# Performance work log

Hardware: AMD Instinct MI355X
Metric: run time of the kernel (lower is better)

The kernel has to match this reference:

```python
import jax, jax.numpy as jnp
import numpy as np

GAMMA = 0.1


def spmm(edge_index, edge_weight, feat, n_nodes):
    # y[dst] += w * feat[src]  -- sparse adjacency @ feat via gather/scatter
    src = edge_index[0]
    dst = edge_index[1]
    msgs = feat[src] * edge_weight[:, None]  # [E, d]
    return jax.ops.segment_sum(msgs, dst, num_segments=n_nodes)


def setup_inputs() -> dict:
    key = jax.random.key(0)
    ks = jax.random.split(key, 12)
    N, F, H, O = 50000, 500, 64, 16
    E, Ek = 1600000, 1000000
    x = jax.random.normal(ks[0], (N, F), dtype=jnp.float32)
    edge_index = jax.random.randint(ks[1], (2, E), 0, N, dtype=jnp.int32)
    edge_weight = jax.random.uniform(ks[2], (E,), dtype=jnp.float32)
    knn_edge_index = jax.random.randint(ks[3], (2, Ek), 0, N, dtype=jnp.int32)
    knn_edge_weight = jax.random.uniform(ks[4], (Ek,), dtype=jnp.float32)
    # glorot-ish scaled params
    W0 = jax.random.normal(ks[5], (F, H), dtype=jnp.float32) * (1.0 / np.sqrt(F))
    W1 = jax.random.normal(ks[6], (H, O), dtype=jnp.float32) * (1.0 / np.sqrt(H))
    score0 = jax.random.normal(ks[7], (F, 1), dtype=jnp.float32) * (1.0 / np.sqrt(F))
    score1 = jax.random.normal(ks[8], (H, 1), dtype=jnp.float32) * (1.0 / np.sqrt(H))
    Dk0 = jax.random.normal(ks[9], (F, 1), dtype=jnp.float32) * (1.0 / np.sqrt(F))
    Dk1 = jax.random.normal(ks[10], (H, 1), dtype=jnp.float32) * (1.0 / np.sqrt(H))
    z = jnp.zeros((1,), dtype=jnp.float32)
    return {
        "x": x, "edge_index": edge_index, "edge_weight": edge_weight,
        "knn_edge_index": knn_edge_index, "knn_edge_weight": knn_edge_weight,
        "W0": W0, "W1": W1,
        "score0": score0, "sbias0": z, "score1": score1, "sbias1": z,
        "Dk0": Dk0, "Dbias0": z, "Dk1": Dk1, "Dbias1": z,
    }


def reference(x, edge_index, edge_weight, knn_edge_index, knn_edge_weight,
              W0, W1, score0, sbias0, score1, sbias1,
              Dk0, Dbias0, Dk1, Dbias1):
    N = x.shape[0]
    layers = [(W0, score0, sbias0, Dk0, Dbias0),
              (W1, score1, sbias1, Dk1, Dbias1)]
    for W, sc, sb, dkw, dkb in layers:
        s = jax.nn.sigmoid(x @ sc + sb)          # [N, 1] gate
        Dk = x @ dkw + dkb                        # [N, 1] degree-like scale
        xW = x @ W                                # shared linear transform
        agg = spmm(edge_index, edge_weight, xW, N)        # GCNConv(x, adj)
        agg_knn = spmm(knn_edge_index, knn_edge_weight, xW, N)  # GCNConv(x, adj_knn)
        # acts are identity (acts=[None] and final act None); dropout off (eval)
        x = s * agg + (1.0 - s) * agg_knn + GAMMA * Dk * xW
    return x
```

## Files before the change

kernel.cpp:

```cpp
#include <hip/hip_runtime.h>
#include <math.h>

#define GAMMA 0.1f

typedef float f32x4 __attribute__((ext_vector_type(4)));
typedef short short4v __attribute__((ext_vector_type(4)));
typedef short short8 __attribute__((ext_vector_type(8)));

static __device__ __forceinline__ unsigned short f2bf(float f) {
  union { float f; unsigned u; } v; v.f = f;
  unsigned r = v.u + 0x7FFF + ((v.u >> 16) & 1);
  return (unsigned short)(r >> 16);
}
static __device__ __forceinline__ float bf2f(unsigned short b) {
  union { unsigned u; float f; } v; v.u = ((unsigned)b) << 16;
  return v.f;
}

__global__ __launch_bounds__(256) void setup_fused(
    int* __restrict__ bcnt2, int ncnt,
    const float* __restrict__ W0, const float* __restrict__ sc0,
    const float* __restrict__ dk0, unsigned short* __restrict__ Bt0, int F,
    const float* __restrict__ W1, const float* __restrict__ sc1,
    const float* __restrict__ dk1, unsigned short* __restrict__ Bt1) {
  int b = blockIdx.x;
  int t = threadIdx.x;
  if (b < 2) {
    int i = b * 256 + t;
    if (i < ncnt) bcnt2[i] = 0;
  } else if (b < 162) {
    int i = (b - 2) * 256 + t;
    int c = i >> 9;
    int k = i & 511;
    float v = 0.f;
    if (k < F) {
      if (c < 64) v = W0[(size_t)k * 64 + c];
      else if (c == 64) v = sc0[k];
      else if (c == 65) v = dk0[k];
    }
    Bt0[(size_t)((k >> 3) * 80 + c) * 8 + (k & 7)] = f2bf(v);
  } else {
    int i = (b - 162) * 256 + t;
    int c = i >> 6;
    int k = i & 63;
    float v;
    if (c < 16) v = W1[(size_t)k * 16 + c];
    else if (c == 16) v = sc1[k];
    else if (c == 17) v = dk1[k];
    else v = 0.f;
    Bt1[(size_t)((k >> 3) * 32 + c) * 8 + (k & 7)] = f2bf(v);
  }
}

template <int CFRAGS, int OUTFRAGS, int COLS>
__global__ __launch_bounds__(256) void mfma_linear_l0(
    const float* __restrict__ A, const unsigned short* __restrict__ Bt3,
    const float* __restrict__ sb, const float* __restrict__ db,
    unsigned short* __restrict__ outW, float* __restrict__ s,
    float* __restrict__ Dk, int N, int Kact) {
  constexpr int KPAD = 512;
  constexpr int KSPLIT = 4, RPB = 16;
  constexpr int KS_PER = (KPAD / 32) / KSPLIT;
  constexpr int H = OUTFRAGS * 16;
  __shared__ unsigned short Ald[RPB * KPAD];
  __shared__ float red[(KSPLIT - 1) * 64 * CFRAGS * 4];

  const int t = threadIdx.x;
  const int rowBase = blockIdx.x * RPB;

#pragma unroll
  for (int it = 0; it < (RPB * KPAD) / (256 * 4); ++it) {
    int li = it * 1024 + t * 4;
    int row = li >> 9;
    int col = li & 511;
    int grow = rowBase + row;
    f32x4 v = (f32x4)0.f;
    if (grow < N && col < Kact)
      v = *(const f32x4*)(A + (size_t)grow * Kact + col);
    short4v b;
#pragma unroll
    for (int j = 0; j < 4; ++j) b[j] = (short)f2bf(v[j]);
    int byte = row * (KPAD * 2) + ((col * 2) ^ ((row & 7) << 4));
    *(short4v*)((char*)Ald + byte) = b;
  }
  __syncthreads();

  const int kslice = t >> 6;
  const int l = t & 63;
  const int kgrp = l >> 4;
  const int lc = l & 15;
  const int lrow = lc;
  const int rowD = rowBase + kgrp * 4;

  f32x4 acc[CFRAGS];
#pragma unroll
  for (int i = 0; i < CFRAGS; ++i) acc[i] = (f32x4)0.f;

  const int rbyte = lrow * (KPAD * 2);
  const int rswz = (lrow & 7) << 4;
#pragma unroll
  for (int kk = 0; kk < KS_PER; ++kk) {
    const int ks = kslice * KS_PER + kk;
    short8 av = *(const short8*)((char*)Ald +
                                 (rbyte + ((ks * 64 + kgrp * 16) ^ rswz)));
    const unsigned short* bbase =
        Bt3 + (size_t)((ks * 4 + kgrp) * COLS + lc) * 8;
#pragma unroll
    for (int fc = 0; fc < CFRAGS; ++fc) {
      short8 bv = *(const short8*)(bbase + fc * 128);
      acc[fc] = __builtin_amdgcn_mfma_f32_16x16x32_bf16(av, bv, acc[fc], 0, 0, 0);
    }
  }

  if (kslice > 0) {
    float* dst = red + ((kslice - 1) * 64 + l) * (CFRAGS * 4);
#pragma unroll
    for (int fc = 0; fc < CFRAGS; ++fc)
#pragma unroll
      for (int r = 0; r < 4; ++r) dst[fc * 4 + r] = acc[fc][r];
  }
  __syncthreads();
  if (kslice == 0) {
#pragma unroll
    for (int s2 = 1; s2 < KSPLIT; ++s2) {
      const float* src2 = red + ((s2 - 1) * 64 + l) * (CFRAGS * 4);
#pragma unroll
      for (int fc = 0; fc < CFRAGS; ++fc)
#pragma unroll
        for (int r = 0; r < 4; ++r) acc[fc][r] += src2[fc * 4 + r];
    }
#pragma unroll
    for (int fc = 0; fc < OUTFRAGS; ++fc) {
#pragma unroll
      for (int r = 0; r < 4; ++r) {
        int gr = rowD + r;
        if (gr < N) outW[(size_t)gr * H + fc * 16 + lc] = f2bf(acc[fc][r]);
      }
    }
    if (lc < 2) {
      f32x4 g = acc[CFRAGS - 1];
#pragma unroll
      for (int r = 0; r < 4; ++r) {
        int gr = rowD + r;
        if (gr < N) {
          if (lc == 0) s[gr] = 1.f / (1.f + expf(-(g[r] + sb[0])));
          else Dk[gr] = g[r] + db[0];
        }
      }
    }
  }
}

template <int KPAD, int CFRAGS, int OUTFRAGS, int COLS>
__global__ __launch_bounds__(256) void mfma_linear_bf(
    const unsigned short* __restrict__ Aptr, const unsigned short* __restrict__ Bt3,
    const float* __restrict__ sb, const float* __restrict__ db,
    unsigned short* __restrict__ outW, float* __restrict__ s,
    float* __restrict__ Dk, int N, int Kact) {
  constexpr int H = OUTFRAGS * 16;
  constexpr int KSPLIT = 2, RG = 2, RPB = 32;
  constexpr int KS_PER = (KPAD / 32) / KSPLIT;
  __shared__ float red[(KSPLIT - 1) * RG * 64 * CFRAGS * 4];

  const int w = threadIdx.x >> 6;
  const int rowgrp = w % RG;
  const int kslice = w / RG;
  const int l = threadIdx.x & 63;
  const int kgrp = l >> 4;
  const int lc = l & 15;
  const int rowA = blockIdx.x * RPB + rowgrp * 16 + lc;
  const int rowD = blockIdx.x * RPB + rowgrp * 16 + kgrp * 4;
  const int rowSafe = (rowA < N) ? rowA : 0;

  f32x4 acc[CFRAGS];
#pragma unroll
  for (int i = 0; i < CFRAGS; ++i) acc[i] = (f32x4)0.f;

#pragma unroll
  for (int kk = 0; kk < KS_PER; ++kk) {
    const int ks = kslice * KS_PER + kk;
    const int kb = ks * 32 + kgrp * 8;
    short8 av = *(const short8*)(Aptr + (size_t)rowSafe * Kact + kb);
    const unsigned short* bbase =
        Bt3 + (size_t)((ks * 4 + kgrp) * COLS + lc) * 8;
#pragma unroll
    for (int fc = 0; fc < CFRAGS; ++fc) {
      short8 bv = *(const short8*)(bbase + fc * 128);
      acc[fc] = __builtin_amdgcn_mfma_f32_16x16x32_bf16(av, bv, acc[fc], 0, 0, 0);
    }
  }

  if (kslice > 0) {
    float* dst = red + ((rowgrp)*64 + l) * (CFRAGS * 4);
#pragma unroll
    for (int fc = 0; fc < CFRAGS; ++fc)
#pragma unroll
      for (int r = 0; r < 4; ++r) dst[fc * 4 + r] = acc[fc][r];
  }
  __syncthreads();
  if (kslice == 0) {
    const float* src2 = red + ((rowgrp)*64 + l) * (CFRAGS * 4);
#pragma unroll
    for (int fc = 0; fc < CFRAGS; ++fc)
#pragma unroll
      for (int r = 0; r < 4; ++r) acc[fc][r] += src2[fc * 4 + r];

#pragma unroll
    for (int fc = 0; fc < OUTFRAGS; ++fc) {
#pragma unroll
      for (int r = 0; r < 4; ++r) {
        int gr = rowD + r;
        if (gr < N) outW[(size_t)gr * H + fc * 16 + lc] = f2bf(acc[fc][r]);
      }
    }
    if (lc < 2) {
      f32x4 g = acc[CFRAGS - 1];
#pragma unroll
      for (int r = 0; r < 4; ++r) {
        int gr = rowD + r;
        if (gr < N) {
          if (lc == 0) s[gr] = 1.f / (1.f + expf(-(g[r] + sb[0])));
          else Dk[gr] = g[r] + db[0];
        }
      }
    }
  }
}

#define BIN_CHUNK 8192

__global__ __launch_bounds__(512) void bucket_count2(
    const int* __restrict__ eiA, int EA, int* __restrict__ bcntA,
    const int* __restrict__ eiK, int EK, int* __restrict__ bcntK, int nchA,
    int* __restrict__ pcnt) {
  const int* ei;
  int E, chunk;
  int* bcnt;
  if (blockIdx.x < nchA) { ei = eiA; E = EA; bcnt = bcntA; chunk = blockIdx.x; }
  else { ei = eiK; E = EK; bcnt = bcntK; chunk = blockIdx.x - nchA; }
  __shared__ int lc[256];
  if (threadIdx.x < 256) lc[threadIdx.x] = 0;
  __syncthreads();
  const int base = chunk * BIN_CHUNK;
  for (int k = threadIdx.x; k < BIN_CHUNK; k += 512) {
    int e = base + k;
    if (e < E) atomicAdd(&lc[ei[E + e] >> 8], 1);
  }
  __syncthreads();
  if (threadIdx.x < 256) {
    int c = lc[threadIdx.x];
    pcnt[blockIdx.x * 256 + threadIdx.x] = c;
    if (c) atomicAdd(&bcnt[threadIdx.x], c);
  }
}

__global__ __launch_bounds__(512) void bucket_scan2(
    int* __restrict__ bcntA, int* __restrict__ boffA, int* __restrict__ gcurA,
    int* __restrict__ bcntK, int* __restrict__ boffK, int* __restrict__ gcurK,
    int nb) {
  int* bcnt = blockIdx.x ? bcntK : bcntA;
  int* boff = blockIdx.x ? boffK : boffA;
  int* gcur = blockIdx.x ? gcurK : gcurA;
  __shared__ int sh[512];
  int t = threadIdx.x;
  int v = (t < nb) ? bcnt[t] : 0;
  sh[t] = v;
  __syncthreads();
  int acc = v;
  for (int off = 1; off < 512; off <<= 1) {
    int xx = (t >= off) ? sh[t - off] : 0;
    __syncthreads();
    acc += xx;
    sh[t] = acc;
    __syncthreads();
  }
  if (t < nb) {
    boff[t] = acc - v;
    gcur[t] = acc - v;
  }
  if (t == nb - 1) boff[nb] = acc;
}

__global__ __launch_bounds__(512) void bin_fill2(
    const int* __restrict__ eiA, const float* __restrict__ ewA, int EA,
    int* __restrict__ gcurA, int2* __restrict__ recA,
    const int* __restrict__ eiK, const float* __restrict__ ewK, int EK,
    int* __restrict__ gcurK, int2* __restrict__ recK, int nchA,
    const int* __restrict__ pcnt) {
  const int* ei;
  const float* ew;
  int E, chunk;
  int* gcur;
  int2* rec;
  if (blockIdx.x < nchA) {
    ei = eiA; ew = ewA; E = EA; gcur = gcurA; rec = recA; chunk = blockIdx.x;
  } else {
    ei = eiK; ew = ewK; E = EK; gcur = gcurK; rec = recK;
    chunk = blockIdx.x - nchA;
  }
  __shared__ int scur[256];
  if (threadIdx.x < 256) {
    int c = pcnt[blockIdx.x * 256 + threadIdx.x];
    scur[threadIdx.x] = c ? atomicAdd(&gcur[threadIdx.x], c) : 0;
  }
  __syncthreads();
  const int base = chunk * BIN_CHUNK;
  for (int k = threadIdx.x; k < BIN_CHUNK; k += 512) {
    int e = base + k;
    if (e < E) {
      int src = ei[e];
      int dst = ei[E + e];
      int pos = atomicAdd(&scur[dst >> 8], 1);
      rec[pos] = make_int2(((dst & 255) << 16) | src, __float_as_int(ew[e]));
    }
  }
}

__global__ __launch_bounds__(512) void tile_sort2(
    const int2* __restrict__ recRawA, const int* __restrict__ boffA,
    unsigned* __restrict__ recSA, int* __restrict__ rpA,
    const int2* __restrict__ recRawK, const int* __restrict__ boffK,
    unsigned* __restrict__ recSK, int* __restrict__ rpK, int N, int nb) {
  const int2* recRaw;
  const int* boff;
  unsigned* recS;
  int* rp;
  int tile;
  if (blockIdx.x < nb) {
    recRaw = recRawA; boff = boffA; recS = recSA; rp = rpA; tile = blockIdx.x;
  } else {
    recRaw = recRawK; boff = boffK; recS = recSK; rp = rpK;
    tile = blockIdx.x - nb;
  }
  __shared__ int cnt[256];
  __shared__ int sc[256];
  __shared__ int cur[256];
  const int lo = boff[tile], hi = boff[tile + 1];
  const int t = threadIdx.x;
  if (t < 256) cnt[t] = 0;
  __syncthreads();
  for (int j = lo + t; j < hi; j += 512)
    atomicAdd(&cnt[recRaw[j].x >> 16], 1);
  __syncthreads();
  if (t < 256) sc[t] = cnt[t];
  __syncthreads();
  for (int off = 1; off < 256; off <<= 1) {
    int v = 0;
    if (t < 256 && t >= off) v = sc[t - off];
    __syncthreads();
    if (t < 256) sc[t] += v;
    __syncthreads();
  }
  if (t < 256) {
    int excl = sc[t] - cnt[t];
    cur[t] = excl;
    int n = tile * 256 + t;
    if (n < N) rp[n] = lo + excl;
  }
  if (tile == nb - 1 && t == 0) rp[N] = hi;
  __syncthreads();
  for (int j = lo + t; j < hi; j += 512) {
    int2 r = recRaw[j];
    int pos = lo + atomicAdd(&cur[r.x >> 16], 1);
    recS[pos] = ((unsigned)f2bf(__int_as_float(r.y)) << 16) |
                (unsigned)(r.x & 0xFFFF);
  }
}

static __device__ __forceinline__ float gather64(
    const int* __restrict__ rp, const unsigned* __restrict__ rec,
    const unsigned short* __restrict__ feat, int n, int h) {
  int b = rp[n], e = rp[n + 1];
  float a[16];
#pragma unroll
  for (int u = 0; u < 16; ++u) a[u] = 0.f;
  int j = b;
  for (; j + 16 <= e; j += 16) {
#pragma unroll
    for (int u = 0; u < 16; ++u) {
      unsigned r = rec[j + u];
      a[u] += bf2f((unsigned short)(r >> 16)) *
              bf2f(feat[(size_t)(r & 0xFFFF) * 64 + h]);
    }
  }
  for (; j + 4 <= e; j += 4) {
#pragma unroll
    for (int u = 0; u < 4; ++u) {
      unsigned r = rec[j + u];
      a[u] += bf2f((unsigned short)(r >> 16)) *
              bf2f(feat[(size_t)(r & 0xFFFF) * 64 + h]);
    }
  }
  for (; j < e; ++j) {
    unsigned r = rec[j];
    a[0] += bf2f((unsigned short)(r >> 16)) *
            bf2f(feat[(size_t)(r & 0xFFFF) * 64 + h]);
  }
  float t0 = ((a[0] + a[1]) + (a[2] + a[3])) + ((a[4] + a[5]) + (a[6] + a[7]));
  float t1 = ((a[8] + a[9]) + (a[10] + a[11])) +
             ((a[12] + a[13]) + (a[14] + a[15]));
  return t0 + t1;
}

__global__ __launch_bounds__(256) void agg_combine64(
    const int* __restrict__ rpA, const unsigned* __restrict__ recA,
    const int* __restrict__ rpK, const unsigned* __restrict__ recK,
    const unsigned short* __restrict__ feat, const float* __restrict__ s,
    const float* __restrict__ Dk, unsigned short* __restrict__ outp, int N) {
  int n = __builtin_amdgcn_readfirstlane((blockIdx.x * 256 + threadIdx.x) >> 6);
  if (n >= N) return;
  int h = threadIdx.x & 63;
  float aA = gather64(rpA, recA, feat, n, h);
  float aK = gather64(rpK, recK, feat, n, h);
  float sv = s[n];
  float res = sv * aA + (1.f - sv) * aK +
              GAMMA * Dk[n] * bf2f(feat[(size_t)n * 64 + h]);
  outp[(size_t)n * 64 + h] = f2bf(res);
}

static __device__ __forceinline__ float gather16(
    const int* __restrict__ rp, const unsigned* __restrict__ rec,
    const unsigned short* __restrict__ feat, int n, int h) {
  int b = rp[n], e = rp[n + 1];
  float a0 = 0.f, a1 = 0.f, a2 = 0.f, a3 = 0.f;
  float a4 = 0.f, a5 = 0.f, a6 = 0.f, a7 = 0.f;
  int j = b;
  for (; j + 8 <= e; j += 8) {
    unsigned q0 = rec[j + 0];
    unsigned q1 = rec[j + 1];
    unsigned q2 = rec[j + 2];
    unsigned q3 = rec[j + 3];
    unsigned q4 = rec[j + 4];
    unsigned q5 = rec[j + 5];
    unsigned q6 = rec[j + 6];
    unsigned q7 = rec[j + 7];
    a0 += bf2f((unsigned short)(q0 >> 16)) *
          bf2f(feat[(size_t)(q0 & 0xFFFF) * 16 + h]);
    a1 += bf2f((unsigned short)(q1 >> 16)) *
          bf2f(feat[(size_t)(q1 & 0xFFFF) * 16 + h]);
    a2 += bf2f((unsigned short)(q2 >> 16)) *
          bf2f(feat[(size_t)(q2 & 0xFFFF) * 16 + h]);
    a3 += bf2f((unsigned short)(q3 >> 16)) *
          bf2f(feat[(size_t)(q3 & 0xFFFF) * 16 + h]);
    a4 += bf2f((unsigned short)(q4 >> 16)) *
          bf2f(feat[(size_t)(q4 & 0xFFFF) * 16 + h]);
    a5 += bf2f((unsigned short)(q5 >> 16)) *
          bf2f(feat[(size_t)(q5 & 0xFFFF) * 16 + h]);
    a6 += bf2f((unsigned short)(q6 >> 16)) *
          bf2f(feat[(size_t)(q6 & 0xFFFF) * 16 + h]);
    a7 += bf2f((unsigned short)(q7 >> 16)) *
          bf2f(feat[(size_t)(q7 & 0xFFFF) * 16 + h]);
  }
  for (; j < e; ++j) {
    unsigned q = rec[j];
    a0 += bf2f((unsigned short)(q >> 16)) *
          bf2f(feat[(size_t)(q & 0xFFFF) * 16 + h]);
  }
  return ((a0 + a1) + (a2 + a3)) + ((a4 + a5) + (a6 + a7));
}

__global__ __launch_bounds__(256) void agg_combine16(
    const int* __restrict__ rpA, const unsigned* __restrict__ recA,
    const int* __restrict__ rpK, const unsigned* __restrict__ recK,
    const unsigned short* __restrict__ feat, const float* __restrict__ s,
    const float* __restrict__ Dk, float* __restrict__ outp, int N) {
  int tid = blockIdx.x * 256 + threadIdx.x;
  int n = tid >> 4;
  int h = tid & 15;
  if (n >= N) return;
  float aA = gather16(rpA, recA, feat, n, h);
  float aK = gather16(rpK, recK, feat, n, h);
  float sv = s[n];
  float res = sv * aA + (1.f - sv) * aK +
              GAMMA * Dk[n] * bf2f(feat[(size_t)n * 16 + h]);
  outp[(size_t)n * 16 + h] = res;
}

extern "C" void kernel_launch(void* const* d_in, const int* in_sizes, int n_in,
                              void* d_out, int out_size, void* d_ws, size_t ws_size,
                              hipStream_t stream) {
  const float* x = (const float*)d_in[0];
  const int* edge_index = (const int*)d_in[1];
  const float* edge_weight = (const float*)d_in[2];
  const int* knn_edge_index = (const int*)d_in[3];
  const float* knn_edge_weight = (const float*)d_in[4];
  const float* W0 = (const float*)d_in[5];
  const float* W1 = (const float*)d_in[6];
  const float* score0 = (const float*)d_in[7];
  const float* sbias0 = (const float*)d_in[8];
  const float* score1 = (const float*)d_in[9];
  const float* sbias1 = (const float*)d_in[10];
  const float* Dk0 = (const float*)d_in[11];
  const float* Dbias0 = (const float*)d_in[12];
  const float* Dk1 = (const float*)d_in[13];
  const float* Dbias1 = (const float*)d_in[14];

  const int F = in_sizes[7];
  const int N = in_sizes[0] / F;
  const int E = in_sizes[2];
  const int Ek = in_sizes[4];
  (void)n_in; (void)ws_size; (void)out_size;

  const int nb = (N + 255) / 256;
  const int nchA = (E + BIN_CHUNK - 1) / BIN_CHUNK;
  const int nchK = (Ek + BIN_CHUNK - 1) / BIN_CHUNK;

  char* cur = (char*)d_ws;
  auto alloc = [&](size_t bytes) {
    char* p = cur;
    cur += (bytes + 255) & ~(size_t)255;
    return (void*)p;
  };
  float* sbuf = (float*)alloc((size_t)N * 4);
  float* dkbuf = (float*)alloc((size_t)N * 4);
  int* bcnt2 = (int*)alloc((size_t)2 * nb * 4);
  int* bcntA = bcnt2;
  int* bcntK = bcnt2 + nb;
  int* boffA = (int*)alloc((size_t)(nb + 1) * 4);
  int* boffK = (int*)alloc((size_t)(nb + 1) * 4);
  int* gcurA = (int*)alloc((size_t)nb * 4);
  int* gcurK = (int*)alloc((size_t)nb * 4);
  int* rpA = (int*)alloc((size_t)(N + 1) * 4);
  int* rpK = (int*)alloc((size_t)(N + 1) * 4);
  int* pcnt = (int*)alloc((size_t)(nchA + nchK) * 256 * 4);
  unsigned* recA = (unsigned*)alloc((size_t)E * 4);
  unsigned* recK = (unsigned*)alloc((size_t)Ek * 4);
  unsigned short* Bt0 = (unsigned short*)alloc((size_t)80 * 512 * 2);
  unsigned short* Bt1 = (unsigned short*)alloc((size_t)32 * 64 * 2);
  char* uni = (char*)alloc((size_t)(E + Ek) * 8);
  int2* recRawA = (int2*)uni;
  int2* recRawK = recRawA + E;
  unsigned short* xWb = (unsigned short*)uni;
  unsigned short* x1b = xWb + (size_t)N * 64;
  unsigned short* xW1b = x1b + (size_t)N * 64;

  const int gemmBlocksL0 = (N + 15) / 16;
  const int gemmBlocksL1 = (N + 31) / 32;
  const int agg64Blocks = (int)(((size_t)N * 64 + 255) / 256);
  const int agg16Blocks = (int)(((size_t)N * 16 + 255) / 256);

  setup_fused<<<170, 256, 0, stream>>>(bcnt2, 2 * nb, W0, score0, Dk0, Bt0, F,
                                       W1, score1, Dk1, Bt1);
  bucket_count2<<<nchA + nchK, 512, 0, stream>>>(edge_index, E, bcntA,
                                                 knn_edge_index, Ek, bcntK,
                                                 nchA, pcnt);
  bucket_scan2<<<2, 512, 0, stream>>>(bcntA, boffA, gcurA, bcntK, boffK,
                                      gcurK, nb);
  bin_fill2<<<nchA + nchK, 512, 0, stream>>>(edge_index, edge_weight, E,
                                             gcurA, recRawA, knn_edge_index,
                                             knn_edge_weight, Ek, gcurK,
                                             recRawK, nchA, pcnt);
  tile_sort2<<<2 * nb, 512, 0, stream>>>(recRawA, boffA, recA, rpA, recRawK,
                                         boffK, recK, rpK, N, nb);
  mfma_linear_l0<5, 4, 80><<<gemmBlocksL0, 256, 0, stream>>>(
      x, Bt0, sbias0, Dbias0, xWb, sbuf, dkbuf, N, F);
  agg_combine64<<<agg64Blocks, 256, 0, stream>>>(rpA, recA, rpK, recK, xWb,
                                                 sbuf, dkbuf, x1b, N);
  mfma_linear_bf<64, 2, 1, 32><<<gemmBlocksL1, 256, 0, stream>>>(
      x1b, Bt1, sbias1, Dbias1, xW1b, sbuf, dkbuf, N, 64);
  agg_combine16<<<agg16Blocks, 256, 0, stream>>>(rpA, recA, rpK, recK, xW1b,
                                                 sbuf, dkbuf, (float*)d_out, N);
}
```

Measured before the change: 169.0 us.

## Replace per-node CSR sort with tile-local LDS fixed-point atomic aggregation

Drops the tile_sort2 pass that built a per-node CSR. The bucketed raw edge records, now in 128-node tiles, are aggregated directly inside 1024-thread blocks. Each block accumulates messages into LDS with integer atomics on fixed-point scaled products, then applies the gate/Dk combine and writes the output. This removes a full sort pass over all edges and its record reads and writes. The cost is LDS atomic contention, fixed-point quantization and overflow risk, larger 8-byte records read twice, and separate allocations instead of the aliased workspace.

Result: slower. 236.1 us (+39.7%).

```diff
diff --git a/kernel.cpp b/kernel.cpp
--- a/kernel.cpp
+++ b/kernel.cpp
@@ -2,6 +2,10 @@
 #include <math.h>
 
 #define GAMMA 0.1f
+#define SCALE0 32768.0f
+#define INV0 (1.0f / 32768.0f)
+#define SCALE1 8192.0f
+#define INV1 (1.0f / 8192.0f)
 
 typedef float f32x4 __attribute__((ext_vector_type(4)));
 typedef short short4v __attribute__((ext_vector_type(4)));
@@ -25,11 +29,11 @@
     const float* __restrict__ dk1, unsigned short* __restrict__ Bt1) {
   int b = blockIdx.x;
   int t = threadIdx.x;
-  if (b < 2) {
+  if (b < 4) {
     int i = b * 256 + t;
     if (i < ncnt) bcnt2[i] = 0;
-  } else if (b < 162) {
-    int i = (b - 2) * 256 + t;
+  } else if (b < 164) {
+    int i = (b - 4) * 256 + t;
     int c = i >> 9;
     int k = i & 511;
     float v = 0.f;
@@ -40,7 +44,7 @@
     }
     Bt0[(size_t)((k >> 3) * 80 + c) * 8 + (k & 7)] = f2bf(v);
   } else {
-    int i = (b - 162) * 256 + t;
+    int i = (b - 164) * 256 + t;
     int c = i >> 6;
     int k = i & 63;
     float v;
@@ -238,18 +242,18 @@
   int* bcnt;
   if (blockIdx.x < nchA) { ei = eiA; E = EA; bcnt = bcntA; chunk = blockIdx.x; }
   else { ei = eiK; E = EK; bcnt = bcntK; chunk = blockIdx.x - nchA; }
-  __shared__ int lc[256];
-  if (threadIdx.x < 256) lc[threadIdx.x] = 0;
+  __shared__ int lc[512];
+  lc[threadIdx.x] = 0;
   __syncthreads();
   const int base = chunk * BIN_CHUNK;
   for (int k = threadIdx.x; k < BIN_CHUNK; k += 512) {
     int e = base + k;
-    if (e < E) atomicAdd(&lc[ei[E + e] >> 8], 1);
-  }
-  __syncthreads();
-  if (threadIdx.x < 256) {
+    if (e < E) atomicAdd(&lc[ei[E + e] >> 7], 1);
+  }
+  __syncthreads();
+  {
     int c = lc[threadIdx.x];
-    pcnt[blockIdx.x * 256 + threadIdx.x] = c;
+    pcnt[blockIdx.x * 512 + threadIdx.x] = c;
     if (c) atomicAdd(&bcnt[threadIdx.x], c);
   }
 }
@@ -298,9 +302,9 @@
     ei = eiK; ew = ewK; E = EK; gcur = gcurK; rec = recK;
     chunk = blockIdx.x - nchA;
   }
-  __shared__ int scur[256];
-  if (threadIdx.x < 256) {
-    int c = pcnt[blockIdx.x * 256 + threadIdx.x];
+  __shared__ int scur[512];
+  {
+    int c = pcnt[blockIdx.x * 512 + threadIdx.x];
     scur[threadIdx.x] = c ? atomicAdd(&gcur[threadIdx.x], c) : 0;
   }
   __syncthreads();
@@ -310,170 +314,180 @@
     if (e < E) {
       int src = ei[e];
       int dst = ei[E + e];
-      int pos = atomicAdd(&scur[dst >> 8], 1);
-      rec[pos] = make_int2(((dst & 255) << 16) | src, __float_as_int(ew[e]));
-    }
-  }
-}
-
-__global__ __launch_bounds__(512) void tile_sort2(
-    const int2* __restrict__ recRawA, const int* __restrict__ boffA,
-    unsigned* __restrict__ recSA, int* __restrict__ rpA,
-    const int2* __restrict__ recRawK, const int* __restrict__ boffK,
-    unsigned* __restrict__ recSK, int* __restrict__ rpK, int N, int nb) {
-  const int2* recRaw;
-  const int* boff;
-  unsigned* recS;
-  int* rp;
-  int tile;
-  if (blockIdx.x < nb) {
-    recRaw = recRawA; boff = boffA; recS = recSA; rp = rpA; tile = blockIdx.x;
-  } else {
-    recRaw = recRawK; boff = boffK; recS = recSK; rp = rpK;
-    tile = blockIdx.x - nb;
-  }
-  __shared__ int cnt[256];
-  __shared__ int sc[256];
-  __shared__ int cur[256];
-  const int lo = boff[tile], hi = boff[tile + 1];
-  const int t = threadIdx.x;
-  if (t < 256) cnt[t] = 0;
-  __syncthreads();
-  for (int j = lo + t; j < hi; j += 512)
-    atomicAdd(&cnt[recRaw[j].x >> 16], 1);
-  __syncthreads();
-  if (t < 256) sc[t] = cnt[t];
-  __syncthreads();
-  for (int off = 1; off < 256; off <<= 1) {
-    int v = 0;
-    if (t < 256 && t >= off) v = sc[t - off];
-    __syncthreads();
-    if (t < 256) sc[t] += v;
-    __syncthreads();
-  }
-  if (t < 256) {
-    int excl = sc[t] - cnt[t];
-    cur[t] = excl;
-    int n = tile * 256 + t;
-    if (n < N) rp[n] = lo + excl;
-  }
-  if (tile == nb - 1 && t == 0) rp[N] = hi;
-  __syncthreads();
-  for (int j = lo + t; j < hi; j += 512) {
-    int2 r = recRaw[j];
-    int pos = lo + atomicAdd(&cur[r.x >> 16], 1);
-    recS[pos] = ((unsigned)f2bf(__int_as_float(r.y)) << 16) |
-                (unsigned)(r.x & 0xFFFF);
-  }
-}
-
-static __device__ __forceinline__ float gather64(
-    const int* __restrict__ rp, const unsigned* __restrict__ rec,
-    const unsigned short* __restrict__ feat, int n, int h) {
-  int b = rp[n], e = rp[n + 1];
-  float a[16];
-#pragma unroll
-  for (int u = 0; u < 16; ++u) a[u] = 0.f;
-  int j = b;
-  for (; j + 16 <= e; j += 16) {
-#pragma unroll
-    for (int u = 0; u < 16; ++u) {
-      unsigned r = rec[j + u];
-      a[u] += bf2f((unsigned short)(r >> 16)) *
-              bf2f(feat[(size_t)(r & 0xFFFF) * 64 + h]);
-    }
-  }
-  for (; j + 4 <= e; j += 4) {
-#pragma unroll
-    for (int u = 0; u < 4; ++u) {
-      unsigned r = rec[j + u];
-      a[u] += bf2f((unsigned short)(r >> 16)) *
-              bf2f(feat[(size_t)(r & 0xFFFF) * 64 + h]);
-    }
-  }
-  for (; j < e; ++j) {
-    unsigned r = rec[j];
-    a[0] += bf2f((unsigned short)(r >> 16)) *
-            bf2f(feat[(size_t)(r & 0xFFFF) * 64 + h]);
-  }
-  float t0 = ((a[0] + a[1]) + (a[2] + a[3])) + ((a[4] + a[5]) + (a[6] + a[7]));
-  float t1 = ((a[8] + a[9]) + (a[10] + a[11])) +
-             ((a[12] + a[13]) + (a[14] + a[15]));
-  return t0 + t1;
-}
-
-__global__ __launch_bounds__(256) void agg_combine64(
-    const int* __restrict__ rpA, const unsigned* __restrict__ recA,
-    const int* __restrict__ rpK, const unsigned* __restrict__ recK,
+      int pos = atomicAdd(&scur[dst >> 7], 1);
+      rec[pos] = make_int2(((dst & 127) << 16) | src, __float_as_int(ew[e]));
+    }
+  }
+}
+
+__global__ __launch_bounds__(1024) void aggfix64(
+    const int2* __restrict__ rawA, const int* __restrict__ boffA,
+    const int2* __restrict__ rawK, const int* __restrict__ boffK,
     const unsigned short* __restrict__ feat, const float* __restrict__ s,
     const float* __restrict__ Dk, unsigned short* __restrict__ outp, int N) {
-  int n = __builtin_amdgcn_readfirstlane((blockIdx.x * 256 + threadIdx.x) >> 6);
-  if (n >= N) return;
-  int h = threadIdx.x & 63;
-  float aA = gather64(rpA, recA, feat, n, h);
-  float aK = gather64(rpK, recK, feat, n, h);
-  float sv = s[n];
-  float res = sv * aA + (1.f - sv) * aK +
-              GAMMA * Dk[n] * bf2f(feat[(size_t)n * 64 + h]);
-  outp[(size_t)n * 64 + h] = f2bf(res);
-}
-
-static __device__ __forceinline__ float gather16(
-    const int* __restrict__ rp, const unsigned* __restrict__ rec,
-    const unsigned short* __restrict__ feat, int n, int h) {
-  int b = rp[n], e = rp[n + 1];
-  float a0 = 0.f, a1 = 0.f, a2 = 0.f, a3 = 0.f;
-  float a4 = 0.f, a5 = 0.f, a6 = 0.f, a7 = 0.f;
-  int j = b;
-  for (; j + 8 <= e; j += 8) {
-    unsigned q0 = rec[j + 0];
-    unsigned q1 = rec[j + 1];
-    unsigned q2 = rec[j + 2];
-    unsigned q3 = rec[j + 3];
-    unsigned q4 = rec[j + 4];
-    unsigned q5 = rec[j + 5];
-    unsigned q6 = rec[j + 6];
-    unsigned q7 = rec[j + 7];
-    a0 += bf2f((unsigned short)(q0 >> 16)) *
-          bf2f(feat[(size_t)(q0 & 0xFFFF) * 16 + h]);
-    a1 += bf2f((unsigned short)(q1 >> 16)) *
-          bf2f(feat[(size_t)(q1 & 0xFFFF) * 16 + h]);
-    a2 += bf2f((unsigned short)(q2 >> 16)) *
-          bf2f(feat[(size_t)(q2 & 0xFFFF) * 16 + h]);
-    a3 += bf2f((unsigned short)(q3 >> 16)) *
-          bf2f(feat[(size_t)(q3 & 0xFFFF) * 16 + h]);
-    a4 += bf2f((unsigned short)(q4 >> 16)) *
-          bf2f(feat[(size_t)(q4 & 0xFFFF) * 16 + h]);
-    a5 += bf2f((unsigned short)(q5 >> 16)) *
-          bf2f(feat[(size_t)(q5 & 0xFFFF) * 16 + h]);
-    a6 += bf2f((unsigned short)(q6 >> 16)) *
-          bf2f(feat[(size_t)(q6 & 0xFFFF) * 16 + h]);
-    a7 += bf2f((unsigned short)(q7 >> 16)) *
-          bf2f(feat[(size_t)(q7 & 0xFFFF) * 16 + h]);
-  }
-  for (; j < e; ++j) {
-    unsigned q = rec[j];
-    a0 += bf2f((unsigned short)(q >> 16)) *
-          bf2f(feat[(size_t)(q & 0xFFFF) * 16 + h]);
-  }
-  return ((a0 + a1) + (a2 + a3)) + ((a4 + a5) + (a6 + a7));
-}
-
-__global__ __launch_bounds__(256) void agg_combine16(
-    const int* __restrict__ rpA, const unsigned* __restrict__ recA,
-    const int* __restrict__ rpK, const unsigned* __restrict__ recK,
+  __shared__ int acc[128 * 64];
+  const int tile = blockIdx.x;
+  const int node0 = tile * 128;
+  const int t = threadIdx.x;
+  const int wid = t >> 6;
+  const int h = t & 63;
+
+#pragma unroll
+  for (int u = 0; u < 8; ++u) acc[t + u * 1024] = 0;
+  __syncthreads();
+
+  {
+    int lo = boffA[tile], hi = boffA[tile + 1];
+    int per = (hi - lo + 15) >> 4;
+    int wb = lo + wid * per;
+    int we = min(wb + per, hi);
+    int j = wb;
+    for (; j + 4 <= we; j += 4) {
+      int2 r0 = rawA[j + 0];
+      int2 r1 = rawA[j + 1];
+      int2 r2 = rawA[j + 2];
+      int2 r3 = rawA[j + 3];
+      float f0 = bf2f(feat[(size_t)(r0.x & 0xFFFF) * 64 + h]);
+      float f1 = bf2f(feat[(size_t)(r1.x & 0xFFFF) * 64 + h]);
+      float f2 = bf2f(feat[(size_t)(r2.x & 0xFFFF) * 64 + h]);
+      float f3 = bf2f(feat[(size_t)(r3.x & 0xFFFF) * 64 + h]);
+      atomicAdd(&acc[((r0.x >> 16) & 127) * 64 + h],
+                __float2int_rn(__int_as_float(r0.y) * f0 * SCALE0));
+      atomicAdd(&acc[((r1.x >> 16) & 127) * 64 + h],
+                __float2int_rn(__int_as_float(r1.y) * f1 * SCALE0));
+      atomicAdd(&acc[((r2.x >> 16) & 127) * 64 + h],
+                __float2int_rn(__int_as_float(r2.y) * f2 * SCALE0));
+      atomicAdd(&acc[((r3.x >> 16) & 127) * 64 + h],
+                __float2int_rn(__int_as_float(r3.y) * f3 * SCALE0));
+    }
+    for (; j < we; ++j) {
+      int2 r = rawA[j];
+      float f = bf2f(feat[(size_t)(r.x & 0xFFFF) * 64 + h]);
+      atomicAdd(&acc[((r.x >> 16) & 127) * 64 + h],
+                __float2int_rn(__int_as_float(r.y) * f * SCALE0));
+    }
+  }
+  __syncthreads();
+
+  float keep[8];
+#pragma unroll
+  for (int u = 0; u < 8; ++u) {
+    int idx = t + u * 1024;
+    int n = node0 + (idx >> 6);
+    keep[u] = (n < N) ? s[n] * (float)acc[idx] * INV0 : 0.f;
+  }
+  __syncthreads();
+#pragma unroll
+  for (int u = 0; u < 8; ++u) acc[t + u * 1024] = 0;
+  __syncthreads();
+
+  {
+    int lo = boffK[tile], hi = boffK[tile + 1];
+    int per = (hi - lo + 15) >> 4;
+    int wb = lo + wid * per;
+    int we = min(wb + per, hi);
+    int j = wb;
+    for (; j + 4 <= we; j += 4) {
+      int2 r0 = rawK[j + 0];
+      int2 r1 = rawK[j + 1];
+      int2 r2 = rawK[j + 2];
+      int2 r3 = rawK[j + 3];
+      float f0 = bf2f(feat[(size_t)(r0.x & 0xFFFF) * 64 + h]);
+      float f1 = bf2f(feat[(size_t)(r1.x & 0xFFFF) * 64 + h]);
+      float f2 = bf2f(feat[(size_t)(r2.x & 0xFFFF) * 64 + h]);
+      float f3 = bf2f(feat[(size_t)(r3.x & 0xFFFF) * 64 + h]);
+      atomicAdd(&acc[((r0.x >> 16) & 127) * 64 + h],
+                __float2int_rn(__int_as_float(r0.y) * f0 * SCALE0));
+      atomicAdd(&acc[((r1.x >> 16) & 127) * 64 + h],
+                __float2int_rn(__int_as_float(r1.y) * f1 * SCALE0));
+      atomicAdd(&acc[((r2.x >> 16) & 127) * 64 + h],
+                __float2int_rn(__int_as_float(r2.y) * f2 * SCALE0));
+      atomicAdd(&acc[((r3.x >> 16) & 127) * 64 + h],
+                __float2int_rn(__int_as_float(r3.y) * f3 * SCALE0));
+    }
+    for (; j < we; ++j) {
+      int2 r = rawK[j];
+      float f = bf2f(feat[(size_t)(r.x & 0xFFFF) * 64 + h]);
+      atomicAdd(&acc[((r.x >> 16) & 127) * 64 + h],
+                __float2int_rn(__int_as_float(r.y) * f * SCALE0));
+    }
+  }
+  __syncthreads();
+
+#pragma unroll
+  for (int u = 0; u < 8; ++u) {
+    int idx = t + u * 1024;
+    int n = node0 + (idx >> 6);
+    int h2 = idx & 63;
+    if (n < N) {
+      float res = keep[u] + (1.f - s[n]) * (float)acc[idx] * INV0 +
+                  GAMMA * Dk[n] * bf2f(feat[(size_t)n * 64 + h2]);
+      outp[(size_t)n * 64 + h2] = f2bf(res);
+    }
+  }
+}
+
+__global__ __launch_bounds__(1024) void aggfix16(
+    const int2* __restrict__ rawA, const int* __restrict__ boffA,
+    const int2* __restrict__ rawK, const int* __restrict__ boffK,
     const unsigned short* __restrict__ feat, const float* __restrict__ s,
     const float* __restrict__ Dk, float* __restrict__ outp, int N) {
-  int tid = blockIdx.x * 256 + threadIdx.x;
-  int n = tid >> 4;
-  int h = tid & 15;
-  if (n >= N) return;
-  float aA = gather16(rpA, recA, feat, n, h);
-  float aK = gather16(rpK, recK, feat, n, h);
-  float sv = s[n];
-  float res = sv * aA + (1.f - sv) * aK +
-              GAMMA * Dk[n] * bf2f(feat[(size_t)n * 16 + h]);
-  outp[(size_t)n * 16 + h] = res;
+  __shared__ int accA[128 * 16];
+  __shared__ int accK[128 * 16];
+  const int tile = blockIdx.x;
+  const int node0 = tile * 128;
+  const int t = threadIdx.x;
+  const int wid = t >> 6;
+  const int lane = t & 63;
+  const int eg = lane >> 4;
+  const int h = lane & 15;
+
+#pragma unroll
+  for (int u = 0; u < 2; ++u) {
+    accA[t + u * 1024] = 0;
+    accK[t + u * 1024] = 0;
+  }
+  __syncthreads();
+
+  {
+    int lo = boffA[tile], hi = boffA[tile + 1];
+    int per = (hi - lo + 15) >> 4;
+    int wb = lo + wid * per;
+    int we = min(wb + per, hi);
+    for (int j = wb + eg; j < we; j += 4) {
+      int2 r = rawA[j];
+      float f = bf2f(feat[(size_t)(r.x & 0xFFFF) * 16 + h]);
+      atomicAdd(&accA[((r.x >> 16) & 127) * 16 + h],
+                __float2int_rn(__int_as_float(r.y) * f * SCALE1));
+    }
+  }
+  {
+    int lo = boffK[tile], hi = boffK[tile + 1];
+    int per = (hi - lo + 15) >> 4;
+    int wb = lo + wid * per;
+    int we = min(wb + per, hi);
+    for (int j = wb + eg; j < we; j += 4) {
+      int2 r = rawK[j];
+      float f = bf2f(feat[(size_t)(r.x & 0xFFFF) * 16 + h]);
+      atomicAdd(&accK[((r.x >> 16) & 127) * 16 + h],
+                __float2int_rn(__int_as_float(r.y) * f * SCALE1));
+    }
+  }
+  __syncthreads();
+
+#pragma unroll
+  for (int u = 0; u < 2; ++u) {
+    int idx = t + u * 1024;
+    int n = node0 + (idx >> 4);
+    int h2 = idx & 15;
+    if (n < N) {
+      float sv = s[n];
+      float res = sv * (float)accA[idx] * INV1 +
+                  (1.f - sv) * (float)accK[idx] * INV1 +
+                  GAMMA * Dk[n] * bf2f(feat[(size_t)n * 16 + h2]);
+      outp[(size_t)n * 16 + h2] = res;
+    }
+  }
 }
 
 extern "C" void kernel_launch(void* const* d_in, const int* in_sizes, int n_in,
@@ -501,7 +515,7 @@
   const int Ek = in_sizes[4];
   (void)n_in; (void)ws_size; (void)out_size;
 
-  const int nb = (N + 255) / 256;
+  const int nb = (N + 127) / 128;
   const int nchA = (E + BIN_CHUNK - 1) / BIN_CHUNK;
   const int nchK = (Ek + BIN_CHUNK - 1) / BIN_CHUNK;
 
@@ -520,26 +534,19 @@
   int* boffK = (int*)alloc((size_t)(nb + 1) * 4);
   int* gcurA = (int*)alloc((size_t)nb * 4);
   int* gcurK = (int*)alloc((size_t)nb * 4);
-  int* rpA = (int*)alloc((size_t)(N + 1) * 4);
-  int* rpK = (int*)alloc((size_t)(N + 1) * 4);
-  int* pcnt = (int*)alloc((size_t)(nchA + nchK) * 256 * 4);
-  unsigned* recA = (unsigned*)alloc((size_t)E * 4);
-  unsigned* recK = (unsigned*)alloc((size_t)Ek * 4);
+  int* pcnt = (int*)alloc((size_t)(nchA + nchK) * 512 * 4);
+  int2* recRawA = (int2*)alloc((size_t)E * 8);
+  int2* recRawK = (int2*)alloc((size_t)Ek * 8);
   unsigned short* Bt0 = (unsigned short*)alloc((size_t)80 * 512 * 2);
   unsigned short* Bt1 = (unsigned short*)alloc((size_t)32 * 64 * 2);
-  char* uni = (char*)alloc((size_t)(E + Ek) * 8);
-  int2* recRawA = (int2*)uni;
-  int2* recRawK = recRawA + E;
-  unsigned short* xWb = (unsigned short*)uni;
-  unsigned short* x1b = xWb + (size_t)N * 64;
-  unsigned short* xW1b = x1b + (size_t)N * 64;
+  unsigned short* xWb = (unsigned short*)alloc((size_t)N * 64 * 2);
+  unsigned short* x1b = (unsigned short*)alloc((size_t)N * 64 * 2);
+  unsigned short* xW1b = (unsigned short*)alloc((size_t)N * 16 * 2);
 
   const int gemmBlocksL0 = (N + 15) / 16;
   const int gemmBlocksL1 = (N + 31) / 32;
-  const int agg64Blocks = (int)(((size_t)N * 64 + 255) / 256);
-  const int agg16Blocks = (int)(((size_t)N * 16 + 255) / 256);
-
-  setup_fused<<<170, 256, 0, stream>>>(bcnt2, 2 * nb, W0, score0, Dk0, Bt0, F,
+
+  setup_fused<<<172, 256, 0, stream>>>(bcnt2, 2 * nb, W0, score0, Dk0, Bt0, F,
                                        W1, score1, Dk1, Bt1);
   bucket_count2<<<nchA + nchK, 512, 0, stream>>>(edge_index, E, bcntA,
                                                  knn_edge_index, Ek, bcntK,
@@ -550,14 +557,12 @@
                                              gcurA, recRawA, knn_edge_index,
                                              knn_edge_weight, Ek, gcurK,
                                              recRawK, nchA, pcnt);
-  tile_sort2<<<2 * nb, 512, 0, stream>>>(recRawA, boffA, recA, rpA, recRawK,
-                                         boffK, recK, rpK, N, nb);
   mfma_linear_l0<5, 4, 80><<<gemmBlocksL0, 256, 0, stream>>>(
       x, Bt0, sbias0, Dbias0, xWb, sbuf, dkbuf, N, F);
-  agg_combine64<<<agg64Blocks, 256, 0, stream>>>(rpA, recA, rpK, recK, xWb,
-                                                 sbuf, dkbuf, x1b, N);
+  aggfix64<<<nb, 1024, 0, stream>>>(recRawA, boffA, recRawK, boffK, xWb,
+                                    sbuf, dkbuf, x1b, N);
   mfma_linear_bf<64, 2, 1, 32><<<gemmBlocksL1, 256, 0, stream>>>(
       x1b, Bt1, sbias1, Dbias1, xW1b, sbuf, dkbuf, N, 64);
-  agg_combine16<<<agg16Blocks, 256, 0, stream>>>(rpA, recA, rpK, recK, xW1b,
-                                                 sbuf, dkbuf, (float*)d_out, N);
-}
+  aggfix16<<<nb, 1024, 0, stream>>>(recRawA, boffA, recRawK, boffK, xW1b,
+                                    sbuf, dkbuf, (float*)d_out, N);
+}
```

## Fuse bucket counting into prep kernel and split aggregation across graph wavefronts

Applied to the files above, without the earlier changes.

Bucket counting now runs inside the setup kernel, and the scan sums per-chunk counts itself, which removes one launch and the global bucket atomics. bin_fill also keeps a per-node degree count with global atomics, so tile_sort can skip its counting pass over the raw records. agg_combine64 now gives the adjacency gather and the kNN gather to separate wavefronts and combines them through shared memory, doubling parallelism per node. In exchange, bin_fill issues millions of global atomics and the aggregation adds a block-level barrier.

Measured after the change: 285.2 us. +68.7%, slower.

```diff
diff --git a/kernel.cpp b/kernel.cpp
--- a/kernel.cpp
+++ b/kernel.cpp
@@ -2,6 +2,7 @@
 #include <math.h>
 
 #define GAMMA 0.1f
+#define BIN_CHUNK 8192
 
 typedef float f32x4 __attribute__((ext_vector_type(4)));
 typedef short short4v __attribute__((ext_vector_type(4)));
@@ -17,19 +18,22 @@
   return v.f;
 }
 
-__global__ __launch_bounds__(256) void setup_fused(
-    int* __restrict__ bcnt2, int ncnt,
+__global__ __launch_bounds__(512) void prep_fused(
+    int* __restrict__ dcnt2, int nzero,
     const float* __restrict__ W0, const float* __restrict__ sc0,
     const float* __restrict__ dk0, unsigned short* __restrict__ Bt0, int F,
     const float* __restrict__ W1, const float* __restrict__ sc1,
-    const float* __restrict__ dk1, unsigned short* __restrict__ Bt1) {
-  int b = blockIdx.x;
-  int t = threadIdx.x;
-  if (b < 2) {
-    int i = b * 256 + t;
-    if (i < ncnt) bcnt2[i] = 0;
-  } else if (b < 162) {
-    int i = (b - 2) * 256 + t;
+    const float* __restrict__ dk1, unsigned short* __restrict__ Bt1,
+    const int* __restrict__ eiA, int EA, const int* __restrict__ eiK, int EK,
+    int nchA, int* __restrict__ pcnt, int ZB) {
+  __shared__ int lc[256];
+  const int b = blockIdx.x;
+  const int t = threadIdx.x;
+  if (b < ZB) {
+    int i = b * 512 + t;
+    if (i < nzero) dcnt2[i] = 0;
+  } else if (b < ZB + 80) {
+    int i = (b - ZB) * 512 + t;
     int c = i >> 9;
     int k = i & 511;
     float v = 0.f;
@@ -39,8 +43,8 @@
       else if (c == 65) v = dk0[k];
     }
     Bt0[(size_t)((k >> 3) * 80 + c) * 8 + (k & 7)] = f2bf(v);
-  } else {
-    int i = (b - 162) * 256 + t;
+  } else if (b < ZB + 84) {
+    int i = (b - ZB - 80) * 512 + t;
     int c = i >> 6;
     int k = i & 63;
     float v;
@@ -49,6 +53,145 @@
     else if (c == 17) v = dk1[k];
     else v = 0.f;
     Bt1[(size_t)((k >> 3) * 32 + c) * 8 + (k & 7)] = f2bf(v);
+  } else {
+    int ci = b - (ZB + 84);
+    const int* ei;
+    int E, chunk;
+    if (ci < nchA) { ei = eiA; E = EA; chunk = ci; }
+    else { ei = eiK; E = EK; chunk = ci - nchA; }
+    if (t < 256) lc[t] = 0;
+    __syncthreads();
+    const int base = chunk * BIN_CHUNK;
+    for (int k = t; k < BIN_CHUNK; k += 512) {
+      int e = base + k;
+      if (e < E) atomicAdd(&lc[ei[E + e] >> 8], 1);
+    }
+    __syncthreads();
+    if (t < 256) pcnt[(size_t)ci * 256 + t] = lc[t];
+  }
+}
+
+__global__ __launch_bounds__(512) void bucket_scan2(
+    const int* __restrict__ pcnt, int nchA, int nchK, int nb,
+    int* __restrict__ boffA, int* __restrict__ gcurA,
+    int* __restrict__ boffK, int* __restrict__ gcurK) {
+  const int* base = blockIdx.x ? (pcnt + (size_t)nchA * 256) : pcnt;
+  const int nch = blockIdx.x ? nchK : nchA;
+  int* boff = blockIdx.x ? boffK : boffA;
+  int* gcur = blockIdx.x ? gcurK : gcurA;
+  __shared__ int sh[512];
+  int t = threadIdx.x;
+  int v = 0;
+  if (t < nb)
+    for (int c = 0; c < nch; ++c) v += base[(size_t)c * 256 + t];
+  sh[t] = v;
+  __syncthreads();
+  int acc = v;
+  for (int off = 1; off < 512; off <<= 1) {
+    int xx = (t >= off) ? sh[t - off] : 0;
+    __syncthreads();
+    acc += xx;
+    sh[t] = acc;
+    __syncthreads();
+  }
+  if (t < nb) {
+    boff[t] = acc - v;
+    gcur[t] = acc - v;
+  }
+  if (t == nb - 1) boff[nb] = acc;
+}
+
+__global__ __launch_bounds__(512) void bin_fill2(
+    const int* __restrict__ eiA, const float* __restrict__ ewA, int EA,
+    int* __restrict__ gcurA, int2* __restrict__ recA,
+    const int* __restrict__ eiK, const float* __restrict__ ewK, int EK,
+    int* __restrict__ gcurK, int2* __restrict__ recK, int nchA,
+    const int* __restrict__ pcnt, int* __restrict__ dcntA,
+    int* __restrict__ dcntK) {
+  const int* ei;
+  const float* ew;
+  int E, chunk;
+  int* gcur;
+  int2* rec;
+  int* dcnt;
+  if (blockIdx.x < nchA) {
+    ei = eiA; ew = ewA; E = EA; gcur = gcurA; rec = recA; dcnt = dcntA;
+    chunk = blockIdx.x;
+  } else {
+    ei = eiK; ew = ewK; E = EK; gcur = gcurK; rec = recK; dcnt = dcntK;
+    chunk = blockIdx.x - nchA;
+  }
+  __shared__ int scur[256];
+  if (threadIdx.x < 256) {
+    int c = pcnt[(size_t)blockIdx.x * 256 + threadIdx.x];
+    scur[threadIdx.x] = c ? atomicAdd(&gcur[threadIdx.x], c) : 0;
+  }
+  __syncthreads();
+  const int base = chunk * BIN_CHUNK;
+  for (int k = threadIdx.x; k < BIN_CHUNK; k += 512) {
+    int e = base + k;
+    if (e < E) {
+      int src = ei[e];
+      int dst = ei[E + e];
+      int pos = atomicAdd(&scur[dst >> 8], 1);
+      rec[pos] = make_int2(((dst & 255) << 16) | src, __float_as_int(ew[e]));
+      atomicAdd(&dcnt[dst], 1);
+    }
+  }
+}
+
+__global__ __launch_bounds__(512) void tile_sort2(
+    const int2* __restrict__ recRawA, const int* __restrict__ boffA,
+    unsigned* __restrict__ recSA, int* __restrict__ rpA,
+    const int* __restrict__ dcntA,
+    const int2* __restrict__ recRawK, const int* __restrict__ boffK,
+    unsigned* __restrict__ recSK, int* __restrict__ rpK,
+    const int* __restrict__ dcntK, int N, int nb) {
+  const int2* recRaw;
+  const int* boff;
+  unsigned* recS;
+  int* rp;
+  const int* dcnt;
+  int tile;
+  if (blockIdx.x < nb) {
+    recRaw = recRawA; boff = boffA; recS = recSA; rp = rpA; dcnt = dcntA;
+    tile = blockIdx.x;
+  } else {
+    recRaw = recRawK; boff = boffK; recS = recSK; rp = rpK; dcnt = dcntK;
+    tile = blockIdx.x - nb;
+  }
+  __shared__ int cnt[256];
+  __shared__ int sc[256];
+  __shared__ int cur[256];
+  const int lo = boff[tile], hi = boff[tile + 1];
+  const int t = threadIdx.x;
+  if (t < 256) {
+    int nn = tile * 256 + t;
+    cnt[t] = (nn < N) ? dcnt[nn] : 0;
+  }
+  __syncthreads();
+  if (t < 256) sc[t] = cnt[t];
+  __syncthreads();
+  for (int off = 1; off < 256; off <<= 1) {
+    int v = 0;
+    if (t < 256 && t >= off) v = sc[t - off];
+    __syncthreads();
+    if (t < 256) sc[t] += v;
+    __syncthreads();
+  }
+  if (t < 256) {
+    int excl = sc[t] - cnt[t];
+    cur[t] = excl;
+    int n = tile * 256 + t;
+    if (n < N) rp[n] = lo + excl;
+  }
+  if (tile == nb - 1 && t == 0) rp[N] = hi;
+  __syncthreads();
+  for (int j = lo + t; j < hi; j += 512) {
+    int2 r = recRaw[j];
+    int pos = lo + atomicAdd(&cur[r.x >> 16], 1);
+    recS[pos] = ((unsigned)f2bf(__int_as_float(r.y)) << 16) |
+                (unsigned)(r.x & 0xFFFF);
   }
 }
 
@@ -227,146 +370,6 @@
   }
 }
 
-#define BIN_CHUNK 8192
-
-__global__ __launch_bounds__(512) void bucket_count2(
-    const int* __restrict__ eiA, int EA, int* __restrict__ bcntA,
-    const int* __restrict__ eiK, int EK, int* __restrict__ bcntK, int nchA,
-    int* __restrict__ pcnt) {
-  const int* ei;
-  int E, chunk;
-  int* bcnt;
-  if (blockIdx.x < nchA) { ei = eiA; E = EA; bcnt = bcntA; chunk = blockIdx.x; }
-  else { ei = eiK; E = EK; bcnt = bcntK; chunk = blockIdx.x - nchA; }
-  __shared__ int lc[256];
-  if (threadIdx.x < 256) lc[threadIdx.x] = 0;
-  __syncthreads();
-  const int base = chunk * BIN_CHUNK;
-  for (int k = threadIdx.x; k < BIN_CHUNK; k += 512) {
-    int e = base + k;
-    if (e < E) atomicAdd(&lc[ei[E + e] >> 8], 1);
-  }
-  __syncthreads();
-  if (threadIdx.x < 256) {
-    int c = lc[threadIdx.x];
-    pcnt[blockIdx.x * 256 + threadIdx.x] = c;
-    if (c) atomicAdd(&bcnt[threadIdx.x], c);
-  }
-}
-
-__global__ __launch_bounds__(512) void bucket_scan2(
-    int* __restrict__ bcntA, int* __restrict__ boffA, int* __restrict__ gcurA,
-    int* __restrict__ bcntK, int* __restrict__ boffK, int* __restrict__ gcurK,
-    int nb) {
-  int* bcnt = blockIdx.x ? bcntK : bcntA;
-  int* boff = blockIdx.x ? boffK : boffA;
-  int* gcur = blockIdx.x ? gcurK : gcurA;
-  __shared__ int sh[512];
-  int t = threadIdx.x;
-  int v = (t < nb) ? bcnt[t] : 0;
-  sh[t] = v;
-  __syncthreads();
-  int acc = v;
-  for (int off = 1; off < 512; off <<= 1) {
-    int xx = (t >= off) ? sh[t - off] : 0;
-    __syncthreads();
-    acc += xx;
-    sh[t] = acc;
-    __syncthreads();
-  }
-  if (t < nb) {
-    boff[t] = acc - v;
-    gcur[t] = acc - v;
-  }
-  if (t == nb - 1) boff[nb] = acc;
-}
-
-__global__ __launch_bounds__(512) void bin_fill2(
-    const int* __restrict__ eiA, const float* __restrict__ ewA, int EA,
-    int* __restrict__ gcurA, int2* __restrict__ recA,
-    const int* __restrict__ eiK, const float* __restrict__ ewK, int EK,
-    int* __restrict__ gcurK, int2* __restrict__ recK, int nchA,
-    const int* __restrict__ pcnt) {
-  const int* ei;
-  const float* ew;
-  int E, chunk;
-  int* gcur;
-  int2* rec;
-  if (blockIdx.x < nchA) {
-    ei = eiA; ew = ewA; E = EA; gcur = gcurA; rec = recA; chunk = blockIdx.x;
-  } else {
-    ei = eiK; ew = ewK; E = EK; gcur = gcurK; rec = recK;
-    chunk = blockIdx.x - nchA;
-  }
-  __shared__ int scur[256];
-  if (threadIdx.x < 256) {
-    int c = pcnt[blockIdx.x * 256 + threadIdx.x];
-    scur[threadIdx.x] = c ? atomicAdd(&gcur[threadIdx.x], c) : 0;
-  }
-  __syncthreads();
-  const int base = chunk * BIN_CHUNK;
-  for (int k = threadIdx.x; k < BIN_CHUNK; k += 512) {
-    int e = base + k;
-    if (e < E) {
-      int src = ei[e];
-      int dst = ei[E + e];
-      int pos = atomicAdd(&scur[dst >> 8], 1);
-      rec[pos] = make_int2(((dst & 255) << 16) | src, __float_as_int(ew[e]));
-    }
-  }
-}
-
-__global__ __launch_bounds__(512) void tile_sort2(
-    const int2* __restrict__ recRawA, const int* __restrict__ boffA,
-    unsigned* __restrict__ recSA, int* __restrict__ rpA,
-    const int2* __restrict__ recRawK, const int* __restrict__ boffK,
-    unsigned* __restrict__ recSK, int* __restrict__ rpK, int N, int nb) {
-  const int2* recRaw;
-  const int* boff;
-  unsigned* recS;
-  int* rp;
-  int tile;
-  if (blockIdx.x < nb) {
-    recRaw = recRawA; boff = boffA; recS = recSA; rp = rpA; tile = blockIdx.x;
-  } else {
-    recRaw = recRawK; boff = boffK; recS = recSK; rp = rpK;
-    tile = blockIdx.x - nb;
-  }
-  __shared__ int cnt[256];
-  __shared__ int sc[256];
-  __shared__ int cur[256];
-  const int lo = boff[tile], hi = boff[tile + 1];
-  const int t = threadIdx.x;
-  if (t < 256) cnt[t] = 0;
-  __syncthreads();
-  for (int j = lo + t; j < hi; j += 512)
-    atomicAdd(&cnt[recRaw[j].x >> 16], 1);
-  __syncthreads();
-  if (t < 256) sc[t] = cnt[t];
-  __syncthreads();
-  for (int off = 1; off < 256; off <<= 1) {
-    int v = 0;
-    if (t < 256 && t >= off) v = sc[t - off];
-    __syncthreads();
-    if (t < 256) sc[t] += v;
-    __syncthreads();
-  }
-  if (t < 256) {
-    int excl = sc[t] - cnt[t];
-    cur[t] = excl;
-    int n = tile * 256 + t;
-    if (n < N) rp[n] = lo + excl;
-  }
-  if (tile == nb - 1 && t == 0) rp[N] = hi;
-  __syncthreads();
-  for (int j = lo + t; j < hi; j += 512) {
-    int2 r = recRaw[j];
-    int pos = lo + atomicAdd(&cur[r.x >> 16], 1);
-    recS[pos] = ((unsigned)f2bf(__int_as_float(r.y)) << 16) |
-                (unsigned)(r.x & 0xFFFF);
-  }
-}
-
 static __device__ __forceinline__ float gather64(
     const int* __restrict__ rp, const unsigned* __restrict__ rec,
     const unsigned short* __restrict__ feat, int n, int h) {
@@ -407,15 +410,28 @@
     const int* __restrict__ rpK, const unsigned* __restrict__ recK,
     const unsigned short* __restrict__ feat, const float* __restrict__ s,
     const float* __restrict__ Dk, unsigned short* __restrict__ outp, int N) {
-  int n = __builtin_amdgcn_readfirstlane((blockIdx.x * 256 + threadIdx.x) >> 6);
-  if (n >= N) return;
-  int h = threadIdx.x & 63;
-  float aA = gather64(rpA, recA, feat, n, h);
-  float aK = gather64(rpK, recK, feat, n, h);
-  float sv = s[n];
-  float res = sv * aA + (1.f - sv) * aK +
-              GAMMA * Dk[n] * bf2f(feat[(size_t)n * 64 + h]);
-  outp[(size_t)n * 64 + h] = f2bf(res);
+  __shared__ float part[2][64];
+  const int t = threadIdx.x;
+  const int wid = t >> 6;
+  const int h = t & 63;
+  const int slot = wid >> 1;
+  const int graph = wid & 1;
+  int n = __builtin_amdgcn_readfirstlane(blockIdx.x * 2 + slot);
+
+  float mine = 0.f;
+  if (n < N)
+    mine = graph ? gather64(rpK, recK, feat, n, h)
+                 : gather64(rpA, recA, feat, n, h);
+  if (graph) part[slot][h] = mine;
+  __syncthreads();
+  if (n < N && graph == 0) {
+    float aA = mine;
+    float aK = part[slot][h];
+    float sv = s[n];
+    float res = sv * aA + (1.f - sv) * aK +
+                GAMMA * Dk[n] * bf2f(feat[(size_t)n * 64 + h]);
+    outp[(size_t)n * 64 + h] = f2bf(res);
+  }
 }
 
 static __device__ __forceinline__ float gather16(
@@ -504,6 +520,7 @@
   const int nb = (N + 255) / 256;
   const int nchA = (E + BIN_CHUNK - 1) / BIN_CHUNK;
   const int nchK = (Ek + BIN_CHUNK - 1) / BIN_CHUNK;
+  const int ZB = (2 * N + 511) / 512;
 
   char* cur = (char*)d_ws;
   auto alloc = [&](size_t bytes) {
@@ -513,9 +530,9 @@
   };
   float* sbuf = (float*)alloc((size_t)N * 4);
   float* dkbuf = (float*)alloc((size_t)N * 4);
-  int* bcnt2 = (int*)alloc((size_t)2 * nb * 4);
-  int* bcntA = bcnt2;
-  int* bcntK = bcnt2 + nb;
+  int* dcnt2 = (int*)alloc((size_t)2 * N * 4);
+  int* dcntA = dcnt2;
+  int* dcntK = dcnt2 + N;
   int* boffA = (int*)alloc((size_t)(nb + 1) * 4);
   int* boffK = (int*)alloc((size_t)(nb + 1) * 4);
   int* gcurA = (int*)alloc((size_t)nb * 4);
@@ -536,22 +553,22 @@
 
   const int gemmBlocksL0 = (N + 15) / 16;
   const int gemmBlocksL1 = (N + 31) / 32;
-  const int agg64Blocks = (int)(((size_t)N * 64 + 255) / 256);
+  const int agg64Blocks = (N + 1) / 2;
   const int agg16Blocks = (int)(((size_t)N * 16 + 255) / 256);
 
-  setup_fused<<<170, 256, 0, stream>>>(bcnt2, 2 * nb, W0, score0, Dk0, Bt0, F,
-                                       W1, score1, Dk1, Bt1);
-  bucket_count2<<<nchA + nchK, 512, 0, stream>>>(edge_index, E, bcntA,
-                                                 knn_edge_index, Ek, bcntK,
-                                                 nchA, pcnt);
-  bucket_scan2<<<2, 512, 0, stream>>>(bcntA, boffA, gcurA, bcntK, boffK,
-                                      gcurK, nb);
+  prep_fused<<<ZB + 84 + nchA + nchK, 512, 0, stream>>>(
+      dcnt2, 2 * N, W0, score0, Dk0, Bt0, F, W1, score1, Dk1, Bt1,
+      edge_index, E, knn_edge_index, Ek, nchA, pcnt, ZB);
+  bucket_scan2<<<2, 512, 0, stream>>>(pcnt, nchA, nchK, nb, boffA, gcurA,
+                                      boffK, gcurK);
   bin_fill2<<<nchA + nchK, 512, 0, stream>>>(edge_index, edge_weight, E,
                                              gcurA, recRawA, knn_edge_index,
                                              knn_edge_weight, Ek, gcurK,
-                                             recRawK, nchA, pcnt);
-  tile_sort2<<<2 * nb, 512, 0, stream>>>(recRawA, boffA, recA, rpA, recRawK,
-                                         boffK, recK, rpK, N, nb);
+                                             recRawK, nchA, pcnt, dcntA,
+                                             dcntK);
+  tile_sort2<<<2 * nb, 512, 0, stream>>>(recRawA, boffA, recA, rpA, dcntA,
+                                         recRawK, boffK, recK, rpK, dcntK, N,
+                                         nb);
   mfma_linear_l0<5, 4, 80><<<gemmBlocksL0, 256, 0, stream>>>(
       x, Bt0, sbias0, Dbias0, xWb, sbuf, dkbuf, N, F);
   agg_combine64<<<agg64Blocks, 256, 0, stream>>>(rpA, recA, rpK, recK, xWb,
```
